# Kernel tuning notes

Hardware: AMD Instinct MI355X
Metric: run time of the kernel (lower is better)

The kernel has to match this reference:

```python
import jax, jax.numpy as jnp
import numpy as np

N_NODES = 50000
N_GRAPHS = 256
IN_DIM = 128
HID = 128
N_LAYERS = 3
N_EDGES = 800000


def setup_inputs() -> dict:
    key = jax.random.key(0)
    ks = jax.random.split(key, 16)
    x = jax.random.normal(ks[0], (N_NODES, IN_DIM), dtype=jnp.float32)
    edge_index = jax.random.randint(ks[1], (2, N_EDGES), 0, N_NODES, dtype=jnp.int64)
    batch = jnp.sort(jax.random.randint(ks[2], (N_NODES,), 0, N_GRAPHS, dtype=jnp.int64))
    inp = {"x": x, "edge_index": edge_index, "batch": batch}
    # SAGEConv params per PyG: lin_l (bias) applied to mean-aggregated neighbors,
    # lin_r (no bias) applied to the root node feature.
    dims = [(IN_DIM, HID)] + [(HID, HID)] * (N_LAYERS - 1)
    for i, (din, dout) in enumerate(dims):
        s = 1.0 / np.sqrt(din)
        inp[f"Wl{i}"] = jax.random.uniform(ks[3 + 3 * i], (din, dout), jnp.float32, -s, s)
        inp[f"bl{i}"] = jax.random.uniform(ks[4 + 3 * i], (dout,), jnp.float32, -s, s)
        inp[f"Wr{i}"] = jax.random.uniform(ks[5 + 3 * i], (din, dout), jnp.float32, -s, s)
    return inp


def _sage_conv(x, src, dst, Wl, bl, Wr):
    # mean aggregation of source-node messages into destination nodes
    msg = x[src]                                               # [E, d] gather
    agg = jax.ops.segment_sum(msg, dst, num_segments=N_NODES)  # [N, d] scatter-add
    deg = jax.ops.segment_sum(jnp.ones((src.shape[0], 1), x.dtype), dst,
                              num_segments=N_NODES)
    agg = agg / jnp.maximum(deg, 1.0)
    return agg @ Wl + bl + x @ Wr


def reference(x, edge_index, batch, Wl0, bl0, Wr0, Wl1, bl1, Wr1, Wl2, bl2, Wr2):
    src, dst = edge_index[0], edge_index[1]
    params = [(Wl0, bl0, Wr0), (Wl1, bl1, Wr1), (Wl2, bl2, Wr2)]
    h = x
    for Wl, bl, Wr in params:
        h = jax.nn.relu(_sage_conv(h, src, dst, Wl, bl, Wr))
        # dropout is a no-op in eval mode
    # meanmax readout over graph ids
    cnt = jax.ops.segment_sum(jnp.ones((h.shape[0], 1), h.dtype), batch,
                              num_segments=N_GRAPHS)
    g_mean = jax.ops.segment_sum(h, batch, num_segments=N_GRAPHS) / jnp.maximum(cnt, 1.0)
    g_max = jax.ops.segment_max(h, batch, num_segments=N_GRAPHS)
    g_max = jnp.where(jnp.isfinite(g_max), g_max, 0.0)  # empty graphs -> 0
    return jnp.concatenate([g_mean, g_max], axis=-1)    # [G, 2*HID]
```

## Files before the change

kernel.cpp:

```cpp
#include <hip/hip_runtime.h>
#include <hip/hip_bf16.h>
#include <stdint.h>

#define N_NODES  50000
#define N_GRAPHS 256
#define DIM      128
#define N_EDGES  800000
#define K2       256
#define N_STRIPS (N_NODES / 16)
#define PAD_CAP  64
#define NBUCKET  196
#define NCHUNK   256
#define CHUNK    3125

typedef __attribute__((ext_vector_type(8))) short  short8;
typedef __attribute__((ext_vector_type(4))) float  floatx4;

__device__ __forceinline__ ushort f2bf(float f) {
    union { float f; uint32_t u; } c; c.f = f;
    uint32_t u = c.u;
    return (ushort)((u + 0x7fffu + ((u >> 16) & 1u)) >> 16);
}
__device__ __forceinline__ float bf2f(ushort b) {
    union { uint32_t u; float f; } c; c.u = ((uint32_t)b) << 16;
    return c.f;
}

__global__ __launch_bounds__(256) void k_convert_x(const float* __restrict__ x,
                                                   ushort* __restrict__ xb) {
    int i = blockIdx.x * 256 + threadIdx.x;
    const int n4 = N_NODES * DIM / 4;
    if (i < n4) {
        float4 v = ((const float4*)x)[i];
        uint32_t lo = (uint32_t)f2bf(v.x) | ((uint32_t)f2bf(v.y) << 16);
        uint32_t hi = (uint32_t)f2bf(v.z) | ((uint32_t)f2bf(v.w) << 16);
        ((uint2*)xb)[i] = make_uint2(lo, hi);
    }
}

__global__ __launch_bounds__(256) void k_prep_w_all(const float* __restrict__ Wl0, const float* __restrict__ Wr0,
                                                    const float* __restrict__ Wl1, const float* __restrict__ Wr1,
                                                    const float* __restrict__ Wl2, const float* __restrict__ Wr2,
                                                    ushort* __restrict__ Wt) {
    int i = blockIdx.x * 256 + threadIdx.x;
    if (i < 3 * DIM * K2) {
        int layer = i / (DIM * K2);
        int j = i % (DIM * K2);
        int n = j / K2, k = j % K2;
        const float* Wl = (layer == 0) ? Wl0 : (layer == 1) ? Wl1 : Wl2;
        const float* Wr = (layer == 0) ? Wr0 : (layer == 1) ? Wr1 : Wr2;
        float v = (k < DIM) ? Wl[k * DIM + n] : Wr[(k - DIM) * DIM + n];
        Wt[i] = f2bf(v);
    }
}

__global__ __launch_bounds__(256) void k_hist(const int* __restrict__ dst,
                                              int* __restrict__ counts) {
    __shared__ int hist[NBUCKET];
    int t = threadIdx.x, b = blockIdx.x;
    if (t < NBUCKET) hist[t] = 0;
    __syncthreads();
    const int e0 = b * CHUNK;
    for (int i = t; i < CHUNK; i += 256)
        atomicAdd(&hist[dst[e0 + i] >> 8], 1);
    __syncthreads();
    if (t < NBUCKET) counts[b * NBUCKET + t] = hist[t];
}

__global__ __launch_bounds__(256) void k_scan_col(const int* __restrict__ counts,
                                                  int* __restrict__ off,
                                                  int* __restrict__ total) {
    __shared__ int buf[256];
    int t = threadIdx.x, j = blockIdx.x;
    int v = counts[t * NBUCKET + j];
    buf[t] = v;
    __syncthreads();
    #pragma unroll
    for (int d = 1; d < 256; d <<= 1) {
        int x = (t >= d) ? buf[t - d] : 0;
        __syncthreads();
        buf[t] += x;
        __syncthreads();
    }
    off[t * NBUCKET + j] = buf[t] - v;
    if (t == 255) total[j] = buf[255];
}

__global__ __launch_bounds__(256) void k_scan_total(const int* __restrict__ total,
                                                    int* __restrict__ basep) {
    __shared__ int buf[256];
    int t = threadIdx.x;
    int v = (t < NBUCKET) ? total[t] : 0;
    buf[t] = v;
    __syncthreads();
    #pragma unroll
    for (int d = 1; d < 256; d <<= 1) {
        int x = (t >= d) ? buf[t - d] : 0;
        __syncthreads();
        buf[t] += x;
        __syncthreads();
    }
    if (t < NBUCKET) basep[t] = buf[t] - v;
}

__global__ __launch_bounds__(256) void k_scatter(const int* __restrict__ src,
                                                 const int* __restrict__ dst,
                                                 const int* __restrict__ off,
                                                 const int* __restrict__ basep,
                                                 uint32_t* __restrict__ ebuf) {
    __shared__ int cur[NBUCKET];
    int t = threadIdx.x, b = blockIdx.x;
    if (t < NBUCKET) cur[t] = off[b * NBUCKET + t] + basep[t];
    __syncthreads();
    const int e0 = b * CHUNK;
    for (int i = t; i < CHUNK; i += 256) {
        int d = dst[e0 + i];
        int s = src[e0 + i];
        int p = atomicAdd(&cur[d >> 8], 1);
        ebuf[p] = ((uint32_t)(d & 255) << 16) | (uint32_t)s;
    }
}

__global__ __launch_bounds__(256) void k_build(const uint32_t* __restrict__ ebuf,
                                               const int* __restrict__ total,
                                               const int* __restrict__ basep,
                                               int* __restrict__ padded,
                                               int* __restrict__ cnt) {
    __shared__ int lcnt[256];
    int t = threadIdx.x, j = blockIdx.x;
    lcnt[t] = 0;
    __syncthreads();
    int b0 = basep[j], tot = total[j];
    for (int i = t; i < tot; i += 256) {
        uint32_t v = ebuf[b0 + i];
        int dl = (int)(v >> 16);
        int s  = (int)(v & 0xffffu);
        int p  = atomicAdd(&lcnt[dl], 1);
        if (p < PAD_CAP) padded[((size_t)j * 256 + dl) * PAD_CAP + p] = s;
    }
    __syncthreads();
    int node = j * 256 + t;
    if (node < N_NODES) cnt[node] = lcnt[t];
}

__global__ __launch_bounds__(256) void k_sort_adj(int* __restrict__ padded,
                                                  const int* __restrict__ cnt) {
    int wid  = threadIdx.x >> 6;
    int lane = threadIdx.x & 63;
    int node = blockIdx.x * 4 + wid;
    if (node >= N_NODES) return;
    int deg = cnt[node];
    int m   = deg < PAD_CAP ? deg : PAD_CAP;
    int* lst = padded + (size_t)node * PAD_CAP;
    int v = (lane < m) ? lst[lane] : 0x7fffffff;
    #pragma unroll
    for (int k = 2; k <= 64; k <<= 1) {
        #pragma unroll
        for (int j = k >> 1; j > 0; j >>= 1) {
            int other  = __shfl_xor(v, j, 64);
            bool down  = (lane & k) != 0;
            bool lower = (lane & j) == 0;
            v = (lower ^ down) ? min(v, other) : max(v, other);
        }
    }
    if (lane < m) lst[lane] = v;
}

__global__ __launch_bounds__(256) void k_gbounds(const int* __restrict__ batch,
                                                 int* __restrict__ gstart,
                                                 int* __restrict__ gend) {
    int i = blockIdx.x * 256 + threadIdx.x;
    if (i >= N_NODES) return;
    int g = batch[i];
    if (i == 0) gstart[g] = 0;
    int gn = (i + 1 < N_NODES) ? batch[i + 1] : -1;
    if (gn != g) {
        gend[g] = i + 1;
        if (gn >= 0) gstart[gn] = i + 1;
    }
}

template <bool OUT_F32>
__global__ __launch_bounds__(256) void k_layer(const ushort* __restrict__ h_in,
                                               const int* __restrict__ padded,
                                               const int* __restrict__ cnt,
                                               const ushort* __restrict__ Wt,
                                               const float* __restrict__ bias,
                                               ushort* __restrict__ out_bf,
                                               float* __restrict__ out_f) {
    __shared__ ushort sAgg[16 * DIM];
    __shared__ int    sIdx[16 * PAD_CAP];
    __shared__ int    sCnt[16];
    __shared__ int    sChl[4][17];
    __shared__ int    sNch[4];

    int t    = threadIdx.x;
    int wid  = t >> 6;
    int lane = t & 63;
    int r0   = blockIdx.x * 16;
    const uint32_t* hw = (const uint32_t*)h_in;

    ((int4*)sIdx)[t] = ((const int4*)(padded + (size_t)r0 * PAD_CAP))[t];
    if (t < 16) sCnt[t] = cnt[r0 + t];
    __syncthreads();

    if (lane == 0) {
        int n = 0;
        #pragma unroll
        for (int q = 0; q < 4; ++q) {
            int m = min(sCnt[wid * 4 + q], PAD_CAP);
            for (int e0 = 0; e0 < m; e0 += 16)
                sChl[wid][n++] = q | (e0 << 8);
        }
        sNch[wid] = n;
    }
    #pragma unroll
    for (int q = 0; q < 4; ++q) {
        int node = wid * 4 + q;
        if (sCnt[node] == 0) ((uint32_t*)(sAgg + node * DIM))[lane] = 0u;
    }
    int nch = sNch[wid];

    float ax[4] = {0.f, 0.f, 0.f, 0.f};
    float ay[4] = {0.f, 0.f, 0.f, 0.f};
    uint32_t va[16], vb[16];

    auto issue = [&](int ci, uint32_t (&v)[16]) {
        int ch   = sChl[wid][ci];
        int q    = ch & 255, e0 = ch >> 8;
        int node = wid * 4 + q;
        int m    = min(sCnt[node], PAD_CAP);
        const int* lst = sIdx + node * PAD_CAP;
        #pragma unroll
        for (int k = 0; k < 16; ++k) {
            int ek = e0 + k;
            int id = lst[ek < m ? ek : m - 1];
            v[k] = hw[(size_t)id * 64 + lane];
        }
    };
    auto consume = [&](int ci, uint32_t (&v)[16], bool isLast) {
        int ch   = sChl[wid][ci];
        int q    = ch & 255, e0 = ch >> 8;
        int node = wid * 4 + q;
        int deg  = sCnt[node];
        int m    = min(deg, PAD_CAP);
        #pragma unroll
        for (int k = 0; k < 16; ++k) {
            uint32_t w = (e0 + k < m) ? v[k] : 0u;
            ax[k & 3] += __uint_as_float(w << 16);
            ay[k & 3] += __uint_as_float(w & 0xffff0000u);
        }
        bool lastOfNode = isLast || ((sChl[wid][ci + 1] & 255) != q);
        if (lastOfNode) {
            float axs = (ax[0] + ax[1]) + (ax[2] + ax[3]);
            float ays = (ay[0] + ay[1]) + (ay[2] + ay[3]);
            float inv = 1.0f / (float)(deg > 0 ? deg : 1);
            uint32_t o = (uint32_t)f2bf(axs * inv) | ((uint32_t)f2bf(ays * inv) << 16);
            ((uint32_t*)(sAgg + node * DIM))[lane] = o;
            #pragma unroll
            for (int j = 0; j < 4; ++j) { ax[j] = 0.f; ay[j] = 0.f; }
        }
    };

    if (nch > 0) {
        issue(0, va);
        int i = 0;
        while (true) {
            bool hasB = (i + 1) < nch;
            if (hasB) issue(i + 1, vb);
            consume(i, va, !hasB);
            if (!hasB) break;
            bool hasA = (i + 2) < nch;
            if (hasA) issue(i + 2, va);
            consume(i + 1, vb, !hasA);
            if (!hasA) break;
            i += 2;
        }
    }
    __syncthreads();

    int row  = lane & 15;
    int quad = lane >> 4;
    short8 a[8];
    const ushort* srow = sAgg + row * DIM + quad * 8;
    #pragma unroll
    for (int ks = 0; ks < 4; ++ks) a[ks] = *(const short8*)(srow + ks * 32);
    const ushort* hrow = h_in + (size_t)(r0 + row) * DIM + quad * 8;
    #pragma unroll
    for (int ks = 0; ks < 4; ++ks) a[4 + ks] = *(const short8*)(hrow + ks * 32);

    #pragma unroll
    for (int c = 0; c < 2; ++c) {
        int ct  = wid * 2 + c;
        int col = ct * 16 + row;
        const ushort* wrow = Wt + (size_t)col * K2 + quad * 8;
        floatx4 acc = {0.f, 0.f, 0.f, 0.f};
        #pragma unroll
        for (int ks = 0; ks < 8; ++ks) {
            short8 b = *(const short8*)(wrow + ks * 32);
            acc = __builtin_amdgcn_mfma_f32_16x16x32_bf16(a[ks], b, acc, 0, 0, 0);
        }
        float bv = bias[col];
        #pragma unroll
        for (int r = 0; r < 4; ++r) {
            int m = r0 + quad * 4 + r;
            float v = acc[r] + bv;
            v = v > 0.f ? v : 0.f;
            if (OUT_F32) out_f[(size_t)m * DIM + col] = v;
            else         out_bf[(size_t)m * DIM + col] = f2bf(v);
        }
    }
}

__global__ __launch_bounds__(128) void k_readout(const float* __restrict__ h,
                                                 const int* __restrict__ batch,
                                                 float* __restrict__ out) {
    int d  = threadIdx.x;
    int n0 = blockIdx.x * 128;
    int n1 = min(n0 + 128, N_NODES);
    int cur = -1; float sum = 0.f, mx = 0.f;
    for (int i = n0; i < n1; ++i) {
        int g = batch[i];
        if (g != cur) {
            if (cur >= 0) {
                atomicAdd(&out[cur * 2 * DIM + d], sum);
                atomicMax((int*)&out[cur * 2 * DIM + DIM + d], __float_as_int(mx));
            }
            cur = g; sum = 0.f; mx = 0.f;
        }
        float v = h[(size_t)i * DIM + d];
        sum += v; mx = fmaxf(mx, v);
    }
    if (cur >= 0) {
        atomicAdd(&out[cur * 2 * DIM + d], sum);
        atomicMax((int*)&out[cur * 2 * DIM + DIM + d], __float_as_int(mx));
    }
}

__global__ __launch_bounds__(256) void k_finalize(float* __restrict__ out,
                                                  const int* __restrict__ gstart,
                                                  const int* __restrict__ gend) {
    int i = blockIdx.x * 256 + threadIdx.x;
    if (i < N_GRAPHS * DIM) {
        int g = i / DIM, d = i % DIM;
        int c = gend[g] - gstart[g];
        out[g * 2 * DIM + d] /= (float)(c > 0 ? c : 1);
    }
}

extern "C" void kernel_launch(void* const* d_in, const int* in_sizes, int n_in,
                              void* d_out, int out_size, void* d_ws, size_t ws_size,
                              hipStream_t stream) {
    const float* x     = (const float*)d_in[0];
    const int*   ei    = (const int*)d_in[1];
    const int*   src   = ei;
    const int*   dst   = ei + N_EDGES;
    const int*   batch = (const int*)d_in[2];
    const float* Wl[3] = {(const float*)d_in[3], (const float*)d_in[6], (const float*)d_in[9]};
    const float* bl[3] = {(const float*)d_in[4], (const float*)d_in[7], (const float*)d_in[10]};
    const float* Wr[3] = {(const float*)d_in[5], (const float*)d_in[8], (const float*)d_in[11]};
    float* out = (float*)d_out;

    char* base = (char*)d_ws;
    size_t o = 0;
    auto alloc = [&](size_t b) -> char* {
        char* p = base + o;
        o = (o + b + 255) & ~(size_t)255;
        return p;
    };
    int*     gstart = (int*)alloc((size_t)N_GRAPHS * 4);
    int*     gend   = (int*)alloc((size_t)N_GRAPHS * 4);
    size_t   zero_bytes = o;
    int*     cnt    = (int*)alloc((size_t)N_NODES * 4);
    int*     counts = (int*)alloc((size_t)NCHUNK * NBUCKET * 4);
    int*     offs   = (int*)alloc((size_t)NCHUNK * NBUCKET * 4);
    int*     total  = (int*)alloc((size_t)NBUCKET * 4);
    int*     basep  = (int*)alloc((size_t)NBUCKET * 4);
    uint32_t* ebuf  = (uint32_t*)alloc((size_t)N_EDGES * 4);
    int*     padded = (int*)alloc((size_t)N_NODES * PAD_CAP * 4);
    ushort*  xb     = (ushort*)alloc((size_t)N_NODES * DIM * 2);
    ushort*  ha     = (ushort*)alloc((size_t)N_NODES * DIM * 2);
    ushort*  hb     = (ushort*)alloc((size_t)N_NODES * DIM * 2);
    float*   h3     = (float*)alloc((size_t)N_NODES * DIM * 4);
    ushort*  Wt     = (ushort*)alloc((size_t)3 * DIM * K2 * 2);
    (void)ws_size; (void)n_in; (void)in_sizes;

    hipMemsetAsync(base, 0, zero_bytes, stream);
    hipMemsetAsync(d_out, 0, (size_t)out_size * 4, stream);

    k_convert_x<<<(N_NODES * DIM / 4 + 255) / 256, 256, 0, stream>>>(x, xb);
    k_prep_w_all<<<(3 * DIM * K2 + 255) / 256, 256, 0, stream>>>(
        Wl[0], Wr[0], Wl[1], Wr[1], Wl[2], Wr[2], Wt);

    k_hist<<<NCHUNK, 256, 0, stream>>>(dst, counts);
    k_scan_col<<<NBUCKET, 256, 0, stream>>>(counts, offs, total);
    k_scan_total<<<1, 256, 0, stream>>>(total, basep);
    k_scatter<<<NCHUNK, 256, 0, stream>>>(src, dst, offs, basep, ebuf);
    k_build<<<NBUCKET, 256, 0, stream>>>(ebuf, total, basep, padded, cnt);
    k_sort_adj<<<(N_NODES + 3) / 4, 256, 0, stream>>>(padded, cnt);
    k_gbounds<<<(N_NODES + 255) / 256, 256, 0, stream>>>(batch, gstart, gend);

    k_layer<false><<<N_STRIPS, 256, 0, stream>>>(xb, padded, cnt, Wt,              bl[0], ha, nullptr);
    k_layer<false><<<N_STRIPS, 256, 0, stream>>>(ha, padded, cnt, Wt + DIM * K2,   bl[1], hb, nullptr);
    k_layer<true ><<<N_STRIPS, 256, 0, stream>>>(hb, padded, cnt, Wt + 2 * DIM * K2, bl[2], nullptr, h3);

    k_readout<<<(N_NODES + 127) / 128, 128, 0, stream>>>(h3, batch, out);
    k_finalize<<<(N_GRAPHS * DIM + 255) / 256, 256, 0, stream>>>(out, gstart, gend);
}
```

Measured before the change: 348.0 us.

## Fuse setup kernels, build adjacency with direct global atomics, add nontemporal accesses

Merges x conversion, weight prep, graph bounds, the cnt zeroing and the output zeroing into one multi-role kernel, which removes several launches and both memsets. The bucketed histogram/scan/scatter/build pipeline becomes a single kernel that does global atomicAdd on per-node counters and writes straight into the padded adjacency. The layer index loads, layer output stores and readout loads become nontemporal, and readout uses smaller row chunks for more parallelism. The risks are global atomic contention and scattered writes in adjacency building, plus more readout atomics. Atomic ordering can change neighbor order before the sort, but the bitonic sort restores a deterministic order.

```diff
diff --git a/kernel.cpp b/kernel.cpp
--- a/kernel.cpp
+++ b/kernel.cpp
@@ -9,12 +9,11 @@
 #define K2       256
 #define N_STRIPS (N_NODES / 16)
 #define PAD_CAP  64
-#define NBUCKET  196
-#define NCHUNK   256
-#define CHUNK    3125
+#define RO_ROWS  32
 
 typedef __attribute__((ext_vector_type(8))) short  short8;
 typedef __attribute__((ext_vector_type(4))) float  floatx4;
+typedef __attribute__((ext_vector_type(4))) int    intx4;
 
 __device__ __forceinline__ ushort f2bf(float f) {
     union { float f; uint32_t u; } c; c.f = f;
@@ -26,24 +25,28 @@
     return c.f;
 }
 
-__global__ __launch_bounds__(256) void k_convert_x(const float* __restrict__ x,
-                                                   ushort* __restrict__ xb) {
-    int i = blockIdx.x * 256 + threadIdx.x;
-    const int n4 = N_NODES * DIM / 4;
-    if (i < n4) {
+#define MB_CONV 6250
+#define MB_PREPW (MB_CONV + 384)
+#define MB_GB   (MB_PREPW + 196)
+#define MB_CNT  (MB_GB + 196)
+#define MB_OUT  (MB_CNT + 256)
+__global__ __launch_bounds__(256) void k_misc(const float* __restrict__ x, ushort* __restrict__ xb,
+                                              const float* __restrict__ Wl0, const float* __restrict__ Wr0,
+                                              const float* __restrict__ Wl1, const float* __restrict__ Wr1,
+                                              const float* __restrict__ Wl2, const float* __restrict__ Wr2,
+                                              ushort* __restrict__ Wt,
+                                              const int* __restrict__ batch,
+                                              int* __restrict__ gstart, int* __restrict__ gend,
+                                              int* __restrict__ cnt, float* __restrict__ out) {
+    int b = blockIdx.x, t = threadIdx.x;
+    if (b < MB_CONV) {
+        int i = b * 256 + t;
         float4 v = ((const float4*)x)[i];
         uint32_t lo = (uint32_t)f2bf(v.x) | ((uint32_t)f2bf(v.y) << 16);
         uint32_t hi = (uint32_t)f2bf(v.z) | ((uint32_t)f2bf(v.w) << 16);
         ((uint2*)xb)[i] = make_uint2(lo, hi);
-    }
-}
-
-__global__ __launch_bounds__(256) void k_prep_w_all(const float* __restrict__ Wl0, const float* __restrict__ Wr0,
-                                                    const float* __restrict__ Wl1, const float* __restrict__ Wr1,
-                                                    const float* __restrict__ Wl2, const float* __restrict__ Wr2,
-                                                    ushort* __restrict__ Wt) {
-    int i = blockIdx.x * 256 + threadIdx.x;
-    if (i < 3 * DIM * K2) {
+    } else if (b < MB_PREPW) {
+        int i = (b - MB_CONV) * 256 + t;
         int layer = i / (DIM * K2);
         int j = i % (DIM * K2);
         int n = j / K2, k = j % K2;
@@ -51,96 +54,36 @@
         const float* Wr = (layer == 0) ? Wr0 : (layer == 1) ? Wr1 : Wr2;
         float v = (k < DIM) ? Wl[k * DIM + n] : Wr[(k - DIM) * DIM + n];
         Wt[i] = f2bf(v);
-    }
-}
-
-__global__ __launch_bounds__(256) void k_hist(const int* __restrict__ dst,
-                                              int* __restrict__ counts) {
-    __shared__ int hist[NBUCKET];
-    int t = threadIdx.x, b = blockIdx.x;
-    if (t < NBUCKET) hist[t] = 0;
-    __syncthreads();
-    const int e0 = b * CHUNK;
-    for (int i = t; i < CHUNK; i += 256)
-        atomicAdd(&hist[dst[e0 + i] >> 8], 1);
-    __syncthreads();
-    if (t < NBUCKET) counts[b * NBUCKET + t] = hist[t];
-}
-
-__global__ __launch_bounds__(256) void k_scan_col(const int* __restrict__ counts,
-                                                  int* __restrict__ off,
-                                                  int* __restrict__ total) {
-    __shared__ int buf[256];
-    int t = threadIdx.x, j = blockIdx.x;
-    int v = counts[t * NBUCKET + j];
-    buf[t] = v;
-    __syncthreads();
-    #pragma unroll
-    for (int d = 1; d < 256; d <<= 1) {
-        int x = (t >= d) ? buf[t - d] : 0;
-        __syncthreads();
-        buf[t] += x;
-        __syncthreads();
-    }
-    off[t * NBUCKET + j] = buf[t] - v;
-    if (t == 255) total[j] = buf[255];
-}
-
-__global__ __launch_bounds__(256) void k_scan_total(const int* __restrict__ total,
-                                                    int* __restrict__ basep) {
-    __shared__ int buf[256];
-    int t = threadIdx.x;
-    int v = (t < NBUCKET) ? total[t] : 0;
-    buf[t] = v;
-    __syncthreads();
-    #pragma unroll
-    for (int d = 1; d < 256; d <<= 1) {
-        int x = (t >= d) ? buf[t - d] : 0;
-        __syncthreads();
-        buf[t] += x;
-        __syncthreads();
-    }
-    if (t < NBUCKET) basep[t] = buf[t] - v;
-}
-
-__global__ __launch_bounds__(256) void k_scatter(const int* __restrict__ src,
-                                                 const int* __restrict__ dst,
-                                                 const int* __restrict__ off,
-                                                 const int* __restrict__ basep,
-                                                 uint32_t* __restrict__ ebuf) {
-    __shared__ int cur[NBUCKET];
-    int t = threadIdx.x, b = blockIdx.x;
-    if (t < NBUCKET) cur[t] = off[b * NBUCKET + t] + basep[t];
-    __syncthreads();
-    const int e0 = b * CHUNK;
-    for (int i = t; i < CHUNK; i += 256) {
-        int d = dst[e0 + i];
-        int s = src[e0 + i];
-        int p = atomicAdd(&cur[d >> 8], 1);
-        ebuf[p] = ((uint32_t)(d & 255) << 16) | (uint32_t)s;
-    }
-}
-
-__global__ __launch_bounds__(256) void k_build(const uint32_t* __restrict__ ebuf,
-                                               const int* __restrict__ total,
-                                               const int* __restrict__ basep,
-                                               int* __restrict__ padded,
-                                               int* __restrict__ cnt) {
-    __shared__ int lcnt[256];
-    int t = threadIdx.x, j = blockIdx.x;
-    lcnt[t] = 0;
-    __syncthreads();
-    int b0 = basep[j], tot = total[j];
-    for (int i = t; i < tot; i += 256) {
-        uint32_t v = ebuf[b0 + i];
-        int dl = (int)(v >> 16);
-        int s  = (int)(v & 0xffffu);
-        int p  = atomicAdd(&lcnt[dl], 1);
-        if (p < PAD_CAP) padded[((size_t)j * 256 + dl) * PAD_CAP + p] = s;
-    }
-    __syncthreads();
-    int node = j * 256 + t;
-    if (node < N_NODES) cnt[node] = lcnt[t];
+    } else if (b < MB_GB) {
+        int i = (b - MB_PREPW) * 256 + t;
+        if (i < N_NODES) {
+            int g = batch[i];
+            if (i == 0) gstart[g] = 0;
+            int gn = (i + 1 < N_NODES) ? batch[i + 1] : -1;
+            if (gn != g) {
+                gend[g] = i + 1;
+                if (gn >= 0) gstart[gn] = i + 1;
+            }
+        }
+    } else if (b < MB_CNT) {
+        int i = (b - MB_GB) * 256 + t;
+        if (i < N_NODES) cnt[i] = 0;
+    } else {
+        int i = (b - MB_CNT) * 256 + t;
+        if (i < N_GRAPHS * 2 * DIM) out[i] = 0.f;
+    }
+}
+
+__global__ __launch_bounds__(256) void k_build_direct(const int* __restrict__ src,
+                                                      const int* __restrict__ dst,
+                                                      int* __restrict__ cnt,
+                                                      int* __restrict__ padded) {
+    int i = blockIdx.x * 256 + threadIdx.x;
+    if (i < N_EDGES) {
+        int d = dst[i], s = src[i];
+        int p = atomicAdd(&cnt[d], 1);
+        if (p < PAD_CAP) padded[(size_t)d * PAD_CAP + p] = s;
+    }
 }
 
 __global__ __launch_bounds__(256) void k_sort_adj(int* __restrict__ padded,
@@ -164,20 +107,6 @@
         }
     }
     if (lane < m) lst[lane] = v;
-}
-
-__global__ __launch_bounds__(256) void k_gbounds(const int* __restrict__ batch,
-                                                 int* __restrict__ gstart,
-                                                 int* __restrict__ gend) {
-    int i = blockIdx.x * 256 + threadIdx.x;
-    if (i >= N_NODES) return;
-    int g = batch[i];
-    if (i == 0) gstart[g] = 0;
-    int gn = (i + 1 < N_NODES) ? batch[i + 1] : -1;
-    if (gn != g) {
-        gend[g] = i + 1;
-        if (gn >= 0) gstart[gn] = i + 1;
-    }
 }
 
 template <bool OUT_F32>
@@ -200,7 +129,8 @@
     int r0   = blockIdx.x * 16;
     const uint32_t* hw = (const uint32_t*)h_in;
 
-    ((int4*)sIdx)[t] = ((const int4*)(padded + (size_t)r0 * PAD_CAP))[t];
+    ((intx4*)sIdx)[t] = __builtin_nontemporal_load(
+        ((const intx4*)(padded + (size_t)r0 * PAD_CAP)) + t);
     if (t < 16) sCnt[t] = cnt[r0 + t];
     __syncthreads();
 
@@ -306,8 +236,8 @@
             int m = r0 + quad * 4 + r;
             float v = acc[r] + bv;
             v = v > 0.f ? v : 0.f;
-            if (OUT_F32) out_f[(size_t)m * DIM + col] = v;
-            else         out_bf[(size_t)m * DIM + col] = f2bf(v);
+            if (OUT_F32) __builtin_nontemporal_store(v, &out_f[(size_t)m * DIM + col]);
+            else         __builtin_nontemporal_store(f2bf(v), &out_bf[(size_t)m * DIM + col]);
         }
     }
 }
@@ -316,8 +246,8 @@
                                                  const int* __restrict__ batch,
                                                  float* __restrict__ out) {
     int d  = threadIdx.x;
-    int n0 = blockIdx.x * 128;
-    int n1 = min(n0 + 128, N_NODES);
+    int n0 = blockIdx.x * RO_ROWS;
+    int n1 = min(n0 + RO_ROWS, N_NODES);
     int cur = -1; float sum = 0.f, mx = 0.f;
     for (int i = n0; i < n1; ++i) {
         int g = batch[i];
@@ -328,7 +258,7 @@
             }
             cur = g; sum = 0.f; mx = 0.f;
         }
-        float v = h[(size_t)i * DIM + d];
+        float v = __builtin_nontemporal_load(&h[(size_t)i * DIM + d]);
         sum += v; mx = fmaxf(mx, v);
     }
     if (cur >= 0) {
@@ -370,40 +300,24 @@
     };
     int*     gstart = (int*)alloc((size_t)N_GRAPHS * 4);
     int*     gend   = (int*)alloc((size_t)N_GRAPHS * 4);
-    size_t   zero_bytes = o;
     int*     cnt    = (int*)alloc((size_t)N_NODES * 4);
-    int*     counts = (int*)alloc((size_t)NCHUNK * NBUCKET * 4);
-    int*     offs   = (int*)alloc((size_t)NCHUNK * NBUCKET * 4);
-    int*     total  = (int*)alloc((size_t)NBUCKET * 4);
-    int*     basep  = (int*)alloc((size_t)NBUCKET * 4);
-    uint32_t* ebuf  = (uint32_t*)alloc((size_t)N_EDGES * 4);
     int*     padded = (int*)alloc((size_t)N_NODES * PAD_CAP * 4);
     ushort*  xb     = (ushort*)alloc((size_t)N_NODES * DIM * 2);
     ushort*  ha     = (ushort*)alloc((size_t)N_NODES * DIM * 2);
     ushort*  hb     = (ushort*)alloc((size_t)N_NODES * DIM * 2);
     float*   h3     = (float*)alloc((size_t)N_NODES * DIM * 4);
     ushort*  Wt     = (ushort*)alloc((size_t)3 * DIM * K2 * 2);
-    (void)ws_size; (void)n_in; (void)in_sizes;
-
-    hipMemsetAsync(base, 0, zero_bytes, stream);
-    hipMemsetAsync(d_out, 0, (size_t)out_size * 4, stream);
-
-    k_convert_x<<<(N_NODES * DIM / 4 + 255) / 256, 256, 0, stream>>>(x, xb);
-    k_prep_w_all<<<(3 * DIM * K2 + 255) / 256, 256, 0, stream>>>(
-        Wl[0], Wr[0], Wl[1], Wr[1], Wl[2], Wr[2], Wt);
-
-    k_hist<<<NCHUNK, 256, 0, stream>>>(dst, counts);
-    k_scan_col<<<NBUCKET, 256, 0, stream>>>(counts, offs, total);
-    k_scan_total<<<1, 256, 0, stream>>>(total, basep);
-    k_scatter<<<NCHUNK, 256, 0, stream>>>(src, dst, offs, basep, ebuf);
-    k_build<<<NBUCKET, 256, 0, stream>>>(ebuf, total, basep, padded, cnt);
+    (void)ws_size; (void)n_in; (void)in_sizes; (void)out_size;
+
+    k_misc<<<MB_OUT, 256, 0, stream>>>(x, xb, Wl[0], Wr[0], Wl[1], Wr[1], Wl[2], Wr[2],
+                                       Wt, batch, gstart, gend, cnt, out);
+    k_build_direct<<<(N_EDGES + 255) / 256, 256, 0, stream>>>(src, dst, cnt, padded);
     k_sort_adj<<<(N_NODES + 3) / 4, 256, 0, stream>>>(padded, cnt);
-    k_gbounds<<<(N_NODES + 255) / 256, 256, 0, stream>>>(batch, gstart, gend);
-
-    k_layer<false><<<N_STRIPS, 256, 0, stream>>>(xb, padded, cnt, Wt,              bl[0], ha, nullptr);
-    k_layer<false><<<N_STRIPS, 256, 0, stream>>>(ha, padded, cnt, Wt + DIM * K2,   bl[1], hb, nullptr);
+
+    k_layer<false><<<N_STRIPS, 256, 0, stream>>>(xb, padded, cnt, Wt,                bl[0], ha, nullptr);
+    k_layer<false><<<N_STRIPS, 256, 0, stream>>>(ha, padded, cnt, Wt + DIM * K2,     bl[1], hb, nullptr);
     k_layer<true ><<<N_STRIPS, 256, 0, stream>>>(hb, padded, cnt, Wt + 2 * DIM * K2, bl[2], nullptr, h3);
 
-    k_readout<<<(N_NODES + 127) / 128, 128, 0, stream>>>(h3, batch, out);
+    k_readout<<<(N_NODES + RO_ROWS - 1) / RO_ROWS, 128, 0, stream>>>(h3, batch, out);
     k_finalize<<<(N_GRAPHS * DIM + 255) / 256, 256, 0, stream>>>(out, gstart, gend);
 }
```

New measurement: 349.4 us. No clear change (+0.4%).
